# Kernel optimization log

Hardware: AMD Instinct MI355X
Metric: run time of the kernel (lower is better)

The kernel has to match this reference:

```python
import jax, jax.numpy as jnp
import numpy as np

B, S, D, H = 4, 2048, 1024, 16
HD = D // H  # 64


def setup_inputs() -> dict:
    key = jax.random.key(0)
    ks = jax.random.split(key, 11)
    scale = 1.0 / np.sqrt(D)
    inp = {
        "query": jax.random.normal(ks[0], (B, S, D), jnp.float32),
        "key": jax.random.normal(ks[1], (B, S, D), jnp.float32),
        "value": jax.random.normal(ks[2], (B, S, D), jnp.float32),
        "mask": jnp.ones((B, 1, 1, S), jnp.float32),
        "wq": jax.random.normal(ks[3], (D, D), jnp.float32) * scale,
        "bq": jnp.zeros((D,), jnp.float32),
        "wk": jax.random.normal(ks[4], (D, D), jnp.float32) * scale,
        "bk": jnp.zeros((D,), jnp.float32),
        "wv": jax.random.normal(ks[5], (D, D), jnp.float32) * scale,
        "bv": jnp.zeros((D,), jnp.float32),
        "wo": jax.random.normal(ks[6], (D, D), jnp.float32) * scale,
        "bo": jnp.zeros((D,), jnp.float32),
    }
    return inp


def reference(query, key, value, mask, wq, bq, wk, bk, wv, bv, wo, bo):
    b = query.shape[0]
    # Dense QKV projections
    q = query @ wq + bq  # [B,S,D]
    k = key @ wk + bk
    v = value @ wv + bv

    def split_heads(x):
        return x.reshape(b, -1, H, HD).transpose(0, 2, 1, 3)  # [B,H,S,HD]

    q, k, v = split_heads(q), split_heads(k), split_heads(v)
    score = jnp.einsum("bhqd,bhkd->bhqk", q, k) / jnp.sqrt(jnp.float32(HD))
    score = score + (1.0 - mask) * -1e9
    alpha = jax.nn.softmax(score, axis=-1)
    context = jnp.einsum("bhqk,bhkd->bhqd", alpha, v)  # [B,H,S,HD]
    context = context.transpose(0, 2, 1, 3).reshape(b, -1, D)
    return context @ wo + bo
```

## Files before the change

### kernel.cpp

```cpp
#include <hip/hip_runtime.h>

using u16 = unsigned short;
using u32 = unsigned int;

typedef float  f32x4  __attribute__((ext_vector_type(4)));
typedef float  f32x16 __attribute__((ext_vector_type(16)));
typedef u32    u32x4  __attribute__((ext_vector_type(4)));
typedef _Float16 f16;
typedef f16 f16x8 __attribute__((ext_vector_type(8)));

#define DEVI static __device__ __forceinline__

constexpr int S_  = 2048;
constexpr int D_  = 1024;
constexpr int HD_ = 64;
constexpr int SH_ = S_*HD_;
constexpr size_t NE_ = 8192ull*1024ull;

DEVI f32x4 mfma16f(f16x8 a, f16x8 b, f32x4 c){
  return __builtin_amdgcn_mfma_f32_16x16x32_f16(a, b, c, 0, 0, 0);
}
DEVI f32x16 mfma32(f16x8 a, f16x8 b, f32x16 c){
  return __builtin_amdgcn_mfma_f32_32x32x16_f16(a, b, c, 0, 0, 0);
}
DEVI float exp2fast(float x){
#if __has_builtin(__builtin_amdgcn_exp2f)
  return __builtin_amdgcn_exp2f(x);
#else
  float r; asm("v_exp_f32 %0, %1" : "=v"(r) : "v"(x)); return r;
#endif
}
DEVI float rcpfast(float x){
#if __has_builtin(__builtin_amdgcn_rcpf)
  return __builtin_amdgcn_rcpf(x);
#else
  float r; asm("v_rcp_f32 %0, %1" : "=v"(r) : "v"(x)); return r;
#endif
}
DEVI u32 pkh(float a, float b){
  return __builtin_bit_cast(u32, __builtin_amdgcn_cvt_pkrtz(a, b));
}
DEVI void gld16(const void* g, void* l){
  __builtin_amdgcn_global_load_lds(
      (const __attribute__((address_space(1))) u32*)g,
      (__attribute__((address_space(3))) u32*)l, 16, 0, 0);
}
DEVI void gld4(const void* g, void* l){
  __builtin_amdgcn_global_load_lds(
      (const __attribute__((address_space(1))) u32*)g,
      (__attribute__((address_space(3))) u32*)l, 4, 0, 0);
}

__global__ __launch_bounds__(256) void wcvt_k(
    const float* __restrict__ wq, const float* __restrict__ wk,
    const float* __restrict__ wv, const float* __restrict__ wo,
    u16* __restrict__ wt)
{
  int z = blockIdx.z;
  const float* W = (z==0)?wq:(z==1)?wk:(z==2)?wv:wo;
  u16* ot = wt + (size_t)z*D_*D_;
  __shared__ float t[64][65];
  int k0 = blockIdx.y*64, n0 = blockIdx.x*64;
  int tid = threadIdx.x;
#pragma unroll
  for (int i=0;i<4;i++){
    int lin = i*256 + tid;
    int r = lin>>4, c = (lin&15)*4;
    f32x4 v = *reinterpret_cast<const f32x4*>(W + (size_t)(k0+r)*D_ + n0 + c);
    t[r][c+0]=v.x; t[r][c+1]=v.y; t[r][c+2]=v.z; t[r][c+3]=v.w;
  }
  __syncthreads();
  int n = tid>>2, c0 = (tid&3)*16;
  alignas(16) u16 hb[16];
#pragma unroll
  for (int i=0;i<16;i++) hb[i] = __builtin_bit_cast(u16, (f16)t[c0+i][n]);
  size_t off = (size_t)(n0+n)*D_ + k0 + c0;
  *reinterpret_cast<u32x4*>(ot+off)   = *reinterpret_cast<u32x4*>(hb);
  *reinterpret_cast<u32x4*>(ot+off+8) = *reinterpret_cast<u32x4*>(hb+8);
}

__global__ __launch_bounds__(256) void madd_k(const float* __restrict__ mask,
                                              float* __restrict__ madd2)
{
  int i = blockIdx.x*256 + threadIdx.x;
  if (i < 4*S_) madd2[i] = (1.0f - mask[i]) * -1442695040.0f;
}

struct GemmArgs {
  const void* A[3];
  const u16*  Wt[3];
  const float* bias[3];
  float*      outF[3];
  u16*        outH[3];
  float       scale[3];
  int         mode[3];
};

template<bool AF32>
__global__ __launch_bounds__(512, 4) void gemm_k(GemmArgs args)
{
  int z = blockIdx.z;
  const float* __restrict__ Af   = (const float*)args.A[z];
  const u16*   __restrict__ Ah   = (const u16*)args.A[z];
  const u16*   __restrict__ Wt   = args.Wt[z];
  const float* __restrict__ bias = args.bias[z];
  int mode = args.mode[z];
  float sc = args.scale[z];

  constexpr int ABYT = AF32 ? 32768 : 16384;
  constexpr int BUFS = ABYT + 8192;
  constexpr int NBUF = AF32 ? 2 : 3;
  __shared__ __align__(16) unsigned char smem[AF32 ? 81920 : 73728];
  char* sbase = (char*)smem;

  int m0 = blockIdx.x*256, n0 = blockIdx.y*128;
  int tid = threadIdx.x, lane = tid&63, w = tid>>6;
  int wm = (w>>1)*64, wn = (w&1)*64;
  int lr = lane&15, lh = lane>>4;

  int offA[4], offB;
  if constexpr (AF32){
#pragma unroll
    for (int j=0;j<4;j++){
      int chunk = w*4 + j;
      int row = chunk*8 + (lane>>3);
      int g = lane&7;
      offA[j] = row*D_ + ((g ^ (row&7))*4);
    }
  } else {
#pragma unroll
    for (int j=0;j<2;j++){
      int chunk = w*2 + j;
      int row = chunk*16 + (lane>>2);
      int gs = lane&3;
      offA[j] = row*D_ + (((gs - (row>>1)) & 3)*8);
    }
  }
  {
    int row = w*16 + (lane>>2);
    int gs = lane&3;
    offB = row*D_ + (((gs - (row>>1)) & 3)*8);
  }

  f32x4 acc[4][4];
#pragma unroll
  for (int m=0;m<4;m++)
#pragma unroll
    for (int n=0;n<4;n++) acc[m][n] = f32x4{0.f,0.f,0.f,0.f};

  auto STAGE = [&](int buf, int kt){
    char* lA = sbase + buf*BUFS;
    char* lB = lA + ABYT;
    if constexpr (AF32){
      const float* As = Af + (size_t)m0*D_ + kt*32;
#pragma unroll
      for (int j=0;j<4;j++) gld16(As + offA[j], lA + (w*4+j)*1024);
    } else {
      const u16* As = Ah + (size_t)m0*D_ + kt*32;
#pragma unroll
      for (int j=0;j<2;j++) gld16(As + offA[j], lA + (w*2+j)*1024);
    }
    const u16* Bs = Wt + (size_t)n0*D_ + kt*32;
    gld16(Bs + offB, lB + w*1024);
  };

  STAGE(0, 0);
  STAGE(1, 1);
  if constexpr (!AF32) STAGE(2, 2);

  for (int kt=0; kt<32; ++kt){
    int buf = kt - (kt/NBUF)*NBUF;
    if constexpr (AF32){
      if (kt < 31) asm volatile("s_waitcnt vmcnt(5)" ::: "memory");
      else         asm volatile("s_waitcnt vmcnt(0)" ::: "memory");
    } else {
      if (kt < 30)       asm volatile("s_waitcnt vmcnt(6)" ::: "memory");
      else if (kt == 30) asm volatile("s_waitcnt vmcnt(3)" ::: "memory");
      else               asm volatile("s_waitcnt vmcnt(0)" ::: "memory");
    }
    __builtin_amdgcn_s_barrier();

    char* bA = sbase + buf*BUFS;
    char* bB = bA + ABYT;
    f16x8 af[4], bfr[4];
#pragma unroll
    for (int m=0;m<4;m++){
      int row = wm + m*16 + lr;
      if constexpr (AF32){
        f32x4 a0 = *reinterpret_cast<const f32x4*>(bA + row*128 + ((((lh<<1)  ) ^ (row&7))<<4));
        f32x4 a1 = *reinterpret_cast<const f32x4*>(bA + row*128 + ((((lh<<1)|1) ^ (row&7))<<4));
        u32x4 uw;
        uw.x = pkh(a0.x,a0.y); uw.y = pkh(a0.z,a0.w);
        uw.z = pkh(a1.x,a1.y); uw.w = pkh(a1.z,a1.w);
        af[m] = __builtin_bit_cast(f16x8, uw);
      } else {
        af[m] = *reinterpret_cast<const f16x8*>(bA + row*64 + (((lh + (row>>1)) & 3)<<4));
      }
    }
#pragma unroll
    for (int n=0;n<4;n++){
      int row = wn + n*16 + lr;
      bfr[n] = *reinterpret_cast<const f16x8*>(bB + row*64 + (((lh + (row>>1)) & 3)<<4));
    }
    asm volatile("s_waitcnt lgkmcnt(0)" ::: "memory");
    __builtin_amdgcn_sched_barrier(0);
    __builtin_amdgcn_s_barrier();
    if constexpr (AF32){
      if (kt < 30) STAGE(buf, kt+2);
    } else {
      if (kt < 29) STAGE(buf, kt+3);
    }

    __builtin_amdgcn_s_setprio(1);
#pragma unroll
    for (int m=0;m<4;m++)
#pragma unroll
      for (int n=0;n<4;n++)
        acc[m][n] = mfma16f(af[m], bfr[n], acc[m][n]);
    __builtin_amdgcn_s_setprio(0);
  }

  float bsetv[4];
#pragma unroll
  for (int n=0;n<4;n++) bsetv[n] = bias[n0 + wn + n*16 + lr];

  if (mode == 0){
    float* out = args.outF[z];
#pragma unroll
    for (int m=0;m<4;m++)
#pragma unroll
      for (int n=0;n<4;n++)
#pragma unroll
        for (int r=0;r<4;r++){
          int row = m0 + wm + m*16 + lh*4 + r;
          int col = n0 + wn + n*16 + lr;
          out[(size_t)row*D_ + col] = (acc[m][n][r] + bsetv[n])*sc;
        }
  } else if (mode == 1){
    u16* oh = args.outH[z];
#pragma unroll
    for (int m=0;m<4;m++)
#pragma unroll
      for (int n=0;n<4;n++)
#pragma unroll
        for (int r=0;r<4;r++){
          int row = m0 + wm + m*16 + lh*4 + r;
          int col = n0 + wn + n*16 + lr;
          float val = (acc[m][n][r] + bsetv[n])*sc;
          int b = row >> 11, s = row & 2047;
          int hh = col >> 6,  dd = col & 63;
          oh[(size_t)(b*16 + hh)*SH_ + (size_t)s*HD_ + dd] =
              __builtin_bit_cast(u16, (f16)val);
        }
  } else {
    __syncthreads();
    u16* ct = (u16*)sbase;
#pragma unroll
    for (int m=0;m<4;m++)
#pragma unroll
      for (int n=0;n<4;n++)
#pragma unroll
        for (int r=0;r<4;r++){
          int lrow = wm + m*16 + lh*4 + r;
          int lcol = wn + n*16 + lr;
          ct[lrow*132 + lcol] = __builtin_bit_cast(u16, (f16)((acc[m][n][r] + bsetv[n])*sc));
        }
    __syncthreads();
    u16* ovt = args.outH[z];
    int b = m0 >> 11, s0 = m0 & 2047;
    int ch = tid >> 2, quarter = tid & 3;
    int gn = n0 + ch;
    int hh = gn >> 6, dd = gn & 63;
    size_t obase = (size_t)(b*16 + hh)*SH_ + (size_t)dd*S_ + s0 + quarter*64;
#pragma unroll
    for (int i=0;i<8;i++){
      alignas(16) u16 tmp[8];
#pragma unroll
      for (int j=0;j<8;j++) tmp[j] = ct[(quarter*64 + i*8 + j)*132 + ch];
      *reinterpret_cast<u32x4*>(ovt + obase + i*8) = *reinterpret_cast<u32x4*>(tmp);
    }
  }
}

__global__ __launch_bounds__(256, 2) void attn_k(
    const f16* __restrict__ Qf, const f16* __restrict__ Kf,
    const f16* __restrict__ Vt, const float* __restrict__ madd2,
    u16* __restrict__ cf)
{
  constexpr int BUFS = 33280;
  __shared__ __align__(16) unsigned char smem[2*BUFS];
  char* sbase = (char*)smem;

  int flat = blockIdx.x + blockIdx.y*gridDim.x;
  int xcd = flat & 7, ix = flat >> 3;
  int bh = xcd + 8*(ix >> 4);
  int qx = ix & 15;
  int b = bh >> 4, head = bh & 15;

  const f16* Qb = Qf + (size_t)bh*SH_;
  const f16* Kb = Kf + (size_t)bh*SH_;
  const f16* Vb = Vt + (size_t)bh*SH_;
  const float* mb = madd2 + (size_t)b*S_;

  int tid = threadIdx.x, lane = tid&63, w = tid>>6;
  int q31 = lane&31, h = lane>>5;
  int qw = qx*128 + w*32;
  int xorv = (q31&7)<<4;

  f16x8 qb[4];
#pragma unroll
  for (int ks=0;ks<4;ks++)
    qb[ks] = *reinterpret_cast<const f16x8*>(Qb + (size_t)(qw + q31)*HD_ + ks*16 + h*8);

  int offK[4], offV[4];
#pragma unroll
  for (int j=0;j<4;j++){
    int L = (w*4+j)*1024 + lane*16;
    int rK = L>>7;
    int dbyK = (L&127) ^ ((rK&7)<<4);
    offK[j] = rK*HD_ + (dbyK>>1);
    int rV = L>>8;
    int dbyV = (L&255) ^ ((rV&7)<<4);
    offV[j] = rV*S_ + (dbyV>>1);
  }

  u32 one2 = 0x3C003C00u;
  u32x4 onev; onev.x=one2; onev.y=one2; onev.z=one2; onev.w=one2;
  f16x8 vones = __builtin_bit_cast(f16x8, onev);

  f32x16 z16;
#pragma unroll
  for (int r=0;r<16;r++) z16[r] = 0.f;

  f32x16 o[2], ol;
#pragma unroll
  for (int n=0;n<2;n++)
#pragma unroll
    for (int r=0;r<16;r++) o[n][r] = 0.f;
#pragma unroll
  for (int r=0;r<16;r++) ol[r] = 0.f;

  auto STAGE = [&](int buf, int t){
    int kv0 = t*128;
    char* sKb = sbase + buf*BUFS;
    char* sVb = sKb + 16384;
    char* sMb = sKb + 32768;
#pragma unroll
    for (int j=0;j<4;j++)
      gld16(Kb + (size_t)kv0*HD_ + offK[j], sKb + (w*4+j)*1024);
#pragma unroll
    for (int j=0;j<4;j++)
      gld16(Vb + kv0 + offV[j], sVb + (w*4+j)*1024);
    gld4(mb + kv0 + lane, sMb);
    gld4(mb + kv0 + 64 + lane, sMb + 256);
  };

  STAGE(0, 0);
  STAGE(1, 1);

  for (int t=0; t<16; ++t){
    int buf = t&1;
    char* sKb = sbase + buf*BUFS;
    char* sVb = sKb + 16384;
    float* sMb = (float*)(sKb + 32768);

    if (t < 15) asm volatile("s_waitcnt vmcnt(10)" ::: "memory");
    else        asm volatile("s_waitcnt vmcnt(0)"  ::: "memory");
    __builtin_amdgcn_s_barrier();
    __builtin_amdgcn_sched_barrier(0);

    f32x16 stA[2], stB[2];

    __builtin_amdgcn_s_setprio(1);
#pragma unroll
    for (int n=0;n<2;n++){
      int rb = (n*32 + q31)*128;
      f16x8 ka = *reinterpret_cast<const f16x8*>(sKb + ((rb + h*16) ^ xorv));
      stA[n] = mfma32(ka, qb[0], z16);
#pragma unroll
      for (int ks=1;ks<4;ks++){
        ka = *reinterpret_cast<const f16x8*>(sKb + ((rb + ks*32 + h*16) ^ xorv));
        stA[n] = mfma32(ka, qb[ks], stA[n]);
      }
    }
#pragma unroll
    for (int n=0;n<2;n++){
      int rb = (64 + n*32 + q31)*128;
      f16x8 ka = *reinterpret_cast<const f16x8*>(sKb + ((rb + h*16) ^ xorv));
      stB[n] = mfma32(ka, qb[0], z16);
#pragma unroll
      for (int ks=1;ks<4;ks++){
        ka = *reinterpret_cast<const f16x8*>(sKb + ((rb + ks*32 + h*16) ^ xorv));
        stB[n] = mfma32(ka, qb[ks], stB[n]);
      }
    }
    __builtin_amdgcn_s_setprio(0);

    auto SMPV = [&](int sub, f32x16 (&st)[2]){
      float mval = sMb[sub*64 + lane];
      if (__ballot(mval != 0.0f)){
#pragma unroll
        for (int n=0;n<2;n++)
#pragma unroll
          for (int g=0;g<4;g++){
            f32x4 mv = *reinterpret_cast<const f32x4*>(sMb + sub*64 + n*32 + g*8 + h*4);
#pragma unroll
            for (int c=0;c<4;c++) st[n][g*4+c] += mv[c];
          }
      }
#pragma unroll
      for (int n=0;n<2;n++)
#pragma unroll
        for (int r=0;r<16;r++) st[n][r] = exp2fast(st[n][r]);

      f16x8 pa[4];
#pragma unroll
      for (int n=0;n<2;n++){
        u32 x[4], y[4];
#pragma unroll
        for (int T=0;T<4;T++){
          x[T] = pkh(st[n][4*T+0], st[n][4*T+1]);
          y[T] = pkh(st[n][4*T+2], st[n][4*T+3]);
        }
#pragma unroll
        for (int k2=0;k2<2;k2++){
          u32 a0=x[2*k2], b0=x[2*k2+1], a1=y[2*k2], b1=y[2*k2+1];
          asm volatile("v_permlane32_swap_b32 %0, %1" : "+v"(a0), "+v"(b0));
          asm volatile("v_permlane32_swap_b32 %0, %1" : "+v"(a1), "+v"(b1));
          u32x4 wv;
          wv.x = a0;
          wv.y = a1;
          wv.z = b0;
          wv.w = b1;
          pa[2*n+k2] = __builtin_bit_cast(f16x8, wv);
        }
      }

      __builtin_amdgcn_s_setprio(1);
#pragma unroll
      for (int n=0;n<2;n++){
        int rbv = (n*32 + q31)*256 + sub*128;
#pragma unroll
        for (int ks=0;ks<4;ks++){
          f16x8 vbf = *reinterpret_cast<const f16x8*>(sVb + ((rbv + ks*32 + h*16) ^ xorv));
          o[n] = mfma32(pa[ks], vbf, o[n]);
        }
      }
#pragma unroll
      for (int ks=0;ks<4;ks++)
        ol = mfma32(pa[ks], vones, ol);
      __builtin_amdgcn_s_setprio(0);
    };

    SMPV(0, stA);
    SMPV(1, stB);

    asm volatile("s_waitcnt lgkmcnt(0)" ::: "memory");
    __builtin_amdgcn_s_barrier();
    __builtin_amdgcn_sched_barrier(0);
    if (t < 14) STAGE(buf, t+2);
  }

#pragma unroll
  for (int n=0;n<2;n++)
#pragma unroll
    for (int r=0;r<16;r++){
      float inv = rcpfast(ol[r]);
      int s = qw + (r&3) + 8*(r>>2) + 4*h;
      int d = head*HD_ + n*32 + q31;
      cf[((size_t)(b*S_ + s))*D_ + d] = __builtin_bit_cast(u16, (f16)(o[n][r]*inv));
    }
}

extern "C" void kernel_launch(void* const* d_in, const int* in_sizes, int n_in,
                              void* d_out, int out_size, void* d_ws, size_t ws_size,
                              hipStream_t stream)
{
  (void)in_sizes; (void)n_in; (void)out_size;
  const float* query=(const float*)d_in[0];
  const float* key  =(const float*)d_in[1];
  const float* value=(const float*)d_in[2];
  const float* mask =(const float*)d_in[3];
  const float* wq=(const float*)d_in[4];
  const float* bq=(const float*)d_in[5];
  const float* wk=(const float*)d_in[6];
  const float* bk=(const float*)d_in[7];
  const float* wv=(const float*)d_in[8];
  const float* bv=(const float*)d_in[9];
  const float* wo=(const float*)d_in[10];
  const float* bo=(const float*)d_in[11];
  float* out = (float*)d_out;

  const size_t WN = 4ull*1024*1024;
  size_t need = WN*2 + 4*NE_*2 + 8192*4;
  if (ws_size < need) return;

  char* ws = (char*)d_ws;
  u16* wt = (u16*)ws;
  u16* qf = wt + WN;
  u16* kf = qf + NE_;
  u16* vt = kf + NE_;
  u16* cf = vt + NE_;
  float* madd2 = (float*)(cf + NE_);

  const float CSC = 0.18033688011112042f;

  wcvt_k<<<dim3(16,16,4), 256, 0, stream>>>(wq,wk,wv,wo,wt);
  madd_k<<<dim3(32), 256, 0, stream>>>(mask, madd2);

  GemmArgs ga{};
  ga.A[0]=query; ga.A[1]=key; ga.A[2]=value;
  ga.Wt[0]=wt;           ga.Wt[1]=wt+1048576;   ga.Wt[2]=wt+2097152;
  ga.bias[0]=bq; ga.bias[1]=bk; ga.bias[2]=bv;
  ga.scale[0]=CSC; ga.scale[1]=1.0f; ga.scale[2]=1.0f;
  ga.mode[0]=1;  ga.mode[1]=1;  ga.mode[2]=2;
  ga.outH[0]=qf; ga.outH[1]=kf; ga.outH[2]=vt;
  gemm_k<true><<<dim3(32,8,3), 512, 0, stream>>>(ga);

  attn_k<<<dim3(16,64), 256, 0, stream>>>((const f16*)qf,(const f16*)kf,(const f16*)vt,madd2,cf);

  GemmArgs go{};
  go.A[0]=cf;
  go.Wt[0]=wt+3145728;
  go.bias[0]=bo; go.scale[0]=1.0f; go.mode[0]=0; go.outF[0]=out;
  gemm_k<false><<<dim3(32,8,1), 512, 0, stream>>>(go);
}
```

Before: 199.1 us.

## Convert fp32 A tiles to fp16 in registers before staging into LDS

For the fp32-input GEMM path, A tiles are now loaded from global memory into registers, packed to fp16, and written to LDS once per tile, instead of being copied as fp32 into LDS and converted on every fragment read. This halves the LDS footprint for A, so the fp32 path can use the same three-buffer pipeline as the fp16 path, and the main loop is restructured into a ping-pong register schedule. The change trades asynchronous global-to-LDS copies for register round-trips and an explicit vmcnt(0) wait each iteration, which can expose global load latency and raise register pressure.

```diff
diff --git a/kernel.cpp b/kernel.cpp
--- a/kernel.cpp
+++ b/kernel.cpp
@@ -107,10 +107,9 @@
   int mode = args.mode[z];
   float sc = args.scale[z];
 
-  constexpr int ABYT = AF32 ? 32768 : 16384;
+  constexpr int ABYT = 16384;
   constexpr int BUFS = ABYT + 8192;
-  constexpr int NBUF = AF32 ? 2 : 3;
-  __shared__ __align__(16) unsigned char smem[AF32 ? 81920 : 73728];
+  __shared__ __align__(16) unsigned char smem[73728];
   char* sbase = (char*)smem;
 
   int m0 = blockIdx.x*256, n0 = blockIdx.y*128;
@@ -118,23 +117,13 @@
   int wm = (w>>1)*64, wn = (w&1)*64;
   int lr = lane&15, lh = lane>>4;
 
-  int offA[4], offB;
-  if constexpr (AF32){
-#pragma unroll
-    for (int j=0;j<4;j++){
-      int chunk = w*4 + j;
-      int row = chunk*8 + (lane>>3);
-      int g = lane&7;
-      offA[j] = row*D_ + ((g ^ (row&7))*4);
-    }
-  } else {
-#pragma unroll
-    for (int j=0;j<2;j++){
-      int chunk = w*2 + j;
-      int row = chunk*16 + (lane>>2);
-      int gs = lane&3;
-      offA[j] = row*D_ + (((gs - (row>>1)) & 3)*8);
-    }
+  int offA[2], offB;
+#pragma unroll
+  for (int j=0;j<2;j++){
+    int chunk = w*2 + j;
+    int row = chunk*16 + (lane>>2);
+    int gs = lane&3;
+    offA[j] = row*D_ + (((gs - (row>>1)) & 3)*8);
   }
   {
     int row = w*16 + (lane>>2);
@@ -142,60 +131,58 @@
     offB = row*D_ + (((gs - (row>>1)) & 3)*8);
   }
 
+  int arow = w*32 + (lane>>1);
+  const float* Abase = AF32 ? (Af + (size_t)(m0 + arow)*D_ + (lane&1)*16) : nullptr;
+
   f32x4 acc[4][4];
 #pragma unroll
   for (int m=0;m<4;m++)
 #pragma unroll
     for (int n=0;n<4;n++) acc[m][n] = f32x4{0.f,0.f,0.f,0.f};
 
-  auto STAGE = [&](int buf, int kt){
-    char* lA = sbase + buf*BUFS;
-    char* lB = lA + ABYT;
-    if constexpr (AF32){
-      const float* As = Af + (size_t)m0*D_ + kt*32;
-#pragma unroll
-      for (int j=0;j<4;j++) gld16(As + offA[j], lA + (w*4+j)*1024);
-    } else {
-      const u16* As = Ah + (size_t)m0*D_ + kt*32;
-#pragma unroll
-      for (int j=0;j<2;j++) gld16(As + offA[j], lA + (w*2+j)*1024);
-    }
-    const u16* Bs = Wt + (size_t)n0*D_ + kt*32;
-    gld16(Bs + offB, lB + w*1024);
+  auto AISSUE = [&](int kt, f32x4* r){
+#pragma unroll
+    for (int j=0;j<4;j++)
+      r[j] = *reinterpret_cast<const f32x4*>(Abase + kt*32 + j*4);
   };
-
-  STAGE(0, 0);
-  STAGE(1, 1);
-  if constexpr (!AF32) STAGE(2, 2);
-
-  for (int kt=0; kt<32; ++kt){
-    int buf = kt - (kt/NBUF)*NBUF;
-    if constexpr (AF32){
-      if (kt < 31) asm volatile("s_waitcnt vmcnt(5)" ::: "memory");
-      else         asm volatile("s_waitcnt vmcnt(0)" ::: "memory");
-    } else {
-      if (kt < 30)       asm volatile("s_waitcnt vmcnt(6)" ::: "memory");
-      else if (kt == 30) asm volatile("s_waitcnt vmcnt(3)" ::: "memory");
-      else               asm volatile("s_waitcnt vmcnt(0)" ::: "memory");
-    }
-    __builtin_amdgcn_s_barrier();
-
+  auto CONVERT = [&](f32x4* r, char* bufA){
+    u32x4 w0, w1;
+    w0.x = pkh(r[0].x,r[0].y); w0.y = pkh(r[0].z,r[0].w);
+    w0.z = pkh(r[1].x,r[1].y); w0.w = pkh(r[1].z,r[1].w);
+    w1.x = pkh(r[2].x,r[2].y); w1.y = pkh(r[2].z,r[2].w);
+    w1.z = pkh(r[3].x,r[3].y); w1.w = pkh(r[3].z,r[3].w);
+    char* dst = bufA + arow*64;
+    int g0 = (lane&1)*2;
+    *reinterpret_cast<u32x4*>(dst + (((g0   + (arow>>1))&3)<<4)) = w0;
+    *reinterpret_cast<u32x4*>(dst + (((g0+1 + (arow>>1))&3)<<4)) = w1;
+  };
+  auto BSTAGE = [&](int kt){
+    char* lB = sbase + (kt - (kt/3)*3)*BUFS + ABYT;
+    gld16(Wt + (size_t)n0*D_ + kt*32 + offB, lB + w*1024);
+  };
+  auto ASTAGE16 = [&](int kt){
+    char* lA = sbase + (kt - (kt/3)*3)*BUFS;
+    const u16* As = Ah + (size_t)m0*D_ + kt*32;
+#pragma unroll
+    for (int j=0;j<2;j++) gld16(As + offA[j], lA + (w*2+j)*1024);
+  };
+
+  f32x4 ra[4], rb[4];
+
+  auto ITER = [&](int t, f32x4* rc){
+    int buf = t - (t/3)*3;
     char* bA = sbase + buf*BUFS;
     char* bB = bA + ABYT;
+
+    asm volatile("s_waitcnt lgkmcnt(0)" ::: "memory");
+    __builtin_amdgcn_s_barrier();
+    __builtin_amdgcn_sched_barrier(0);
+
     f16x8 af[4], bfr[4];
 #pragma unroll
     for (int m=0;m<4;m++){
       int row = wm + m*16 + lr;
-      if constexpr (AF32){
-        f32x4 a0 = *reinterpret_cast<const f32x4*>(bA + row*128 + ((((lh<<1)  ) ^ (row&7))<<4));
-        f32x4 a1 = *reinterpret_cast<const f32x4*>(bA + row*128 + ((((lh<<1)|1) ^ (row&7))<<4));
-        u32x4 uw;
-        uw.x = pkh(a0.x,a0.y); uw.y = pkh(a0.z,a0.w);
-        uw.z = pkh(a1.x,a1.y); uw.w = pkh(a1.z,a1.w);
-        af[m] = __builtin_bit_cast(f16x8, uw);
-      } else {
-        af[m] = *reinterpret_cast<const f16x8*>(bA + row*64 + (((lh + (row>>1)) & 3)<<4));
-      }
+      af[m] = *reinterpret_cast<const f16x8*>(bA + row*64 + (((lh + (row>>1)) & 3)<<4));
     }
 #pragma unroll
     for (int n=0;n<4;n++){
@@ -205,10 +192,22 @@
     asm volatile("s_waitcnt lgkmcnt(0)" ::: "memory");
     __builtin_amdgcn_sched_barrier(0);
     __builtin_amdgcn_s_barrier();
+
     if constexpr (AF32){
-      if (kt < 30) STAGE(buf, kt+2);
+      if (t < 31){
+        asm volatile("s_waitcnt vmcnt(0)" ::: "memory");
+        int nb = (t+1) - ((t+1)/3)*3;
+        CONVERT(rc, sbase + nb*BUFS);
+      }
+      if (t < 29){
+        AISSUE(t+3, rc);
+        BSTAGE(t+3);
+      }
     } else {
-      if (kt < 29) STAGE(buf, kt+3);
+      if (t < 29){ ASTAGE16(t+3); BSTAGE(t+3); }
+      if (t < 30)       asm volatile("s_waitcnt vmcnt(6)" ::: "memory");
+      else if (t == 30) asm volatile("s_waitcnt vmcnt(3)" ::: "memory");
+      else              asm volatile("s_waitcnt vmcnt(0)" ::: "memory");
     }
 
     __builtin_amdgcn_s_setprio(1);
@@ -218,6 +217,24 @@
       for (int n=0;n<4;n++)
         acc[m][n] = mfma16f(af[m], bfr[n], acc[m][n]);
     __builtin_amdgcn_s_setprio(0);
+  };
+
+  if constexpr (AF32){
+    AISSUE(0, ra); BSTAGE(0);
+    AISSUE(1, rb); BSTAGE(1);
+    CONVERT(ra, sbase);
+    AISSUE(2, ra); BSTAGE(2);
+    asm volatile("s_waitcnt vmcnt(5)" ::: "memory");
+    for (int it=0; it<16; ++it){
+      ITER(2*it,   rb);
+      ITER(2*it+1, ra);
+    }
+  } else {
+    ASTAGE16(0); BSTAGE(0);
+    ASTAGE16(1); BSTAGE(1);
+    ASTAGE16(2); BSTAGE(2);
+    asm volatile("s_waitcnt vmcnt(6)" ::: "memory");
+    for (int t=0; t<32; ++t) ITER(t, ra);
   }
 
   float bsetv[4];
```

Result: slower. 354.8 us (+78.2%).
